# Optimization experiments

Measured on AMD Instinct MI355X. Metric: run time of the kernel, lower is better.

The kernel has to match this reference:

```python
import jax, jax.numpy as jnp
import numpy as np

EMB, NH, NG, T_MAX = 2048, 16, 4, 2048
HD = EMB // NH          # 128
HPG = NH // NG          # 4
B, T = 2, 2048


def _rope_tables(t):
    inv_freq = 1.0 / (10000.0 ** (jnp.arange(0, HD, 2, dtype=jnp.float32) / HD))
    freqs = jnp.outer(jnp.arange(t, dtype=jnp.float32), inv_freq)  # [t, HD//2]
    return jnp.cos(freqs), jnp.sin(freqs)


def _apply_rope(x, cos, sin):
    # x: [..., t, HD], interleaved pairs (0::2 real, 1::2 imag)
    x1 = x[..., 0::2]
    x2 = x[..., 1::2]
    r1 = x1 * cos - x2 * sin
    r2 = x1 * sin + x2 * cos
    return jnp.stack([r1, r2], axis=-1).reshape(x.shape)


def setup_inputs() -> dict:
    key = jax.random.key(0)
    ks = jax.random.split(key, 5)
    s = 0.02
    return {
        "x": jax.random.normal(ks[0], (B, T, EMB), dtype=jnp.float32),
        "Wq": jax.random.normal(ks[1], (EMB, EMB), dtype=jnp.float32) * s,
        "Wk": jax.random.normal(ks[2], (NG * HD, EMB), dtype=jnp.float32) * s,
        "Wv": jax.random.normal(ks[3], (NG * HD, EMB), dtype=jnp.float32) * s,
        "Wo": jax.random.normal(ks[4], (EMB, EMB), dtype=jnp.float32) * s,
    }


def reference(x, Wq, Wk, Wv, Wo):
    b, t, _ = x.shape
    cos, sin = _rope_tables(t)  # [t, HD//2] each; broadcast over batch/heads

    # projections (torch Linear: x @ W.T)
    q = (x @ Wq.T).reshape(b, t, NH, HD).transpose(0, 2, 1, 3)  # [b, NH, t, HD]
    k = (x @ Wk.T).reshape(b, t, NG, HD).transpose(0, 2, 1, 3)  # [b, NG, t, HD]
    v = (x @ Wv.T).reshape(b, t, NG, HD).transpose(0, 2, 1, 3)  # [b, NG, t, HD]

    q = _apply_rope(q, cos, sin)
    k = _apply_rope(k, cos, sin)

    # grouped attention without materializing expanded K/V
    qg = q.reshape(b, NG, HPG, t, HD)                       # [b, g, h, t, d]
    scale = 1.0 / jnp.sqrt(jnp.asarray(HD, dtype=x.dtype))
    scores = jnp.einsum('bghtd,bgsd->bghts', qg, k) * scale  # [b, g, h, t, s]

    causal = jnp.tril(jnp.ones((t, t), dtype=bool))
    scores = jnp.where(causal, scores, jnp.finfo(scores.dtype).min)
    attn = jax.nn.softmax(scores, axis=-1)

    out = jnp.einsum('bghts,bgsd->bghtd', attn, v)           # [b, g, h, t, d]
    out = out.reshape(b, NH, t, HD).transpose(0, 2, 1, 3).reshape(b, t, EMB)
    return out @ Wo.T
```

## Files before the change

kernel.cpp:

```cpp
#include <hip/hip_runtime.h>
#include <stdint.h>
#include <math.h>

#define EMB 2048
#define NHq 16
#define NGk 4
#define HD 128
#define Bb 2
#define Tt 2048
#define MROWS (Bb*Tt)
#define QKVN 3072
#define NQT 32

typedef __bf16 bf16x8 __attribute__((ext_vector_type(8)));
typedef float f32x4 __attribute__((ext_vector_type(4)));
typedef unsigned int u32x4 __attribute__((ext_vector_type(4)));
typedef unsigned short u16;
typedef unsigned int u32;

__device__ __forceinline__ u16 f2bf(float f) {
    unsigned int u = __float_as_uint(f);
    u += 0x7fff + ((u >> 16) & 1);
    return (u16)(u >> 16);
}
__device__ __forceinline__ float bf2f(u16 u) {
    return __uint_as_float(((u32)u) << 16);
}
__device__ __forceinline__ u32 cvt_pk_bf16(float lo, float hi) {
    u32 r;
    asm("v_cvt_pk_bf16_f32 %0, %1, %2" : "=v"(r) : "v"(lo), "v"(hi));
    return r;
}

#define GLOAD_LDS16(g, l) \
    __builtin_amdgcn_global_load_lds((const __attribute__((address_space(1))) void*)(g), \
                                     (__attribute__((address_space(3))) void*)(l), 16, 0, 0)
#define FENCE asm volatile("" ::: "memory")
#define BARRIER { FENCE; __builtin_amdgcn_s_barrier(); FENCE; }
#define VMCNT(n) asm volatile("s_waitcnt vmcnt(" #n ")")

__global__ void cast_bf16_kernel(const float* __restrict__ src, u16* __restrict__ dst, int n4) {
    int i = blockIdx.x * blockDim.x + threadIdx.x;
    if (i < n4) {
        float4 v = reinterpret_cast<const float4*>(src)[i];
        ushort4 o;
        o.x = f2bf(v.x); o.y = f2bf(v.y); o.z = f2bf(v.z); o.w = f2bf(v.w);
        reinterpret_cast<ushort4*>(dst)[i] = o;
    }
}

__global__ void wcast_kernel(const float* __restrict__ Wq, const float* __restrict__ Wk,
                             const float* __restrict__ Wv, const float* __restrict__ Wo,
                             u16* __restrict__ dst) {
    int i = blockIdx.x * blockDim.x + threadIdx.x;
    const float* src; int local;
    if (i < 1048576)      { src = Wq; local = i; }
    else if (i < 1310720) { src = Wk; local = i - 1048576; }
    else if (i < 1572864) { src = Wv; local = i - 1310720; }
    else                  { src = Wo; local = i - 1572864; }
    float4 v = reinterpret_cast<const float4*>(src)[local];
    ushort4 o;
    o.x = f2bf(v.x); o.y = f2bf(v.y); o.z = f2bf(v.z); o.w = f2bf(v.w);
    reinterpret_cast<ushort4*>(dst)[i] = o;
}

__global__ void rope_tables_kernel(float* __restrict__ ctab, float* __restrict__ stab) {
    int t = blockIdx.x, i = threadIdx.x;
    float inv = powf(10000.f, -2.f * (float)i / (float)HD);
    float ang = (float)t * inv;
    ctab[t * 64 + i] = cosf(ang);
    stab[t * 64 + i] = sinf(ang);
}

__global__ void rope_qk_kernel(const u16* __restrict__ lin, const float* __restrict__ ctab,
                               const float* __restrict__ stab, u16* __restrict__ Qb,
                               u16* __restrict__ Kb, float qscale) {
    int i = threadIdx.x;
    int tt = blockIdx.x * 4 + threadIdx.y;
    int hh = blockIdx.y, b = blockIdx.z;
    int coloff; u16* out; float scale;
    if (hh < NHq) { coloff = hh * HD; scale = qscale;
                    out = Qb + (((size_t)(b * NHq + hh)) * Tt + tt) * HD; }
    else { int g = hh - NHq; coloff = EMB + g * HD; scale = 1.f;
           out = Kb + (((size_t)(b * NGk + g)) * Tt + tt) * HD; }
    u32 pair = *reinterpret_cast<const u32*>(&lin[((size_t)(b * Tt + tt)) * QKVN + coloff + 2 * i]);
    float x1 = bf2f((u16)(pair & 0xffff)), x2 = bf2f((u16)(pair >> 16));
    float c = ctab[tt * 64 + i], s = stab[tt * 64 + i];
    ushort2 o;
    o.x = f2bf((x1 * c - x2 * s) * scale);
    o.y = f2bf((x1 * s + x2 * c) * scale);
    *reinterpret_cast<ushort2*>(&out[2 * i]) = o;
}

__global__ void vtrans_kernel(const u16* __restrict__ lin, u16* __restrict__ vt) {
    int tx = threadIdx.x, dy = threadIdx.y;
    int tt = blockIdx.x * 64 + tx;
    int g = blockIdx.y, b = blockIdx.z;
    int ttp = (tt & ~31) | (((tt >> 2) & 3) * 8 + ((tt >> 4) & 1) * 4 + (tt & 3));
    const u16* src = &lin[((size_t)(b * Tt + tt)) * QKVN + EMB + NGk * HD + g * HD];
    u16* dst = &vt[(((size_t)(b * NGk + g)) * HD) * Tt + ttp];
    #pragma unroll
    for (int k = 0; k < 16; ++k) {
        int d = dy + k * 8;
        dst[(size_t)d * Tt] = src[d];
    }
}

template<int OUTBF>
__global__ __launch_bounds__(256) void gemm_bt(const u16* __restrict__ A, const u16* __restrict__ W,
                                               void* __restrict__ Cout, int M, int N, int K) {
    __shared__ u16 Atile[128 * 32];
    __shared__ u16 Btile[128 * 32];
    const int brow = blockIdx.x * 128;
    const int bcol = blockIdx.y * 128;
    const int t = threadIdx.x;
    const int w = t >> 6, l = t & 63;
    const int lr = l & 15, lq = l >> 4;
    const int wr = (w >> 1) * 64, wc = (w & 1) * 64;
    f32x4 acc[4][4] = {};
    const int nkt = K >> 5;
    for (int kt = 0; kt < nkt; ++kt) {
        const int k0 = kt * 32;
        #pragma unroll
        for (int i = 0; i < 2; ++i) {
            int f = i * 256 + t;
            int row = f >> 2, cb = (f & 3) * 8;
            GLOAD_LDS16(A + (size_t)(brow + row) * K + k0 + cb, &Atile[(i * 256 + w * 64) * 8]);
            GLOAD_LDS16(W + (size_t)(bcol + row) * K + k0 + cb, &Btile[(i * 256 + w * 64) * 8]);
        }
        __syncthreads();
        bf16x8 a[4], b[4];
        #pragma unroll
        for (int m = 0; m < 4; ++m)
            a[m] = *reinterpret_cast<const bf16x8*>(&Atile[(wr + m * 16 + lr) * 32 + lq * 8]);
        #pragma unroll
        for (int n = 0; n < 4; ++n)
            b[n] = *reinterpret_cast<const bf16x8*>(&Btile[(wc + n * 16 + lr) * 32 + lq * 8]);
        #pragma unroll
        for (int m = 0; m < 4; ++m)
            #pragma unroll
            for (int n = 0; n < 4; ++n)
                acc[m][n] = __builtin_amdgcn_mfma_f32_16x16x32_bf16(a[m], b[n], acc[m][n], 0, 0, 0);
        __syncthreads();
    }
    #pragma unroll
    for (int m = 0; m < 4; ++m)
        #pragma unroll
        for (int n = 0; n < 4; ++n)
            #pragma unroll
            for (int r = 0; r < 4; ++r) {
                size_t idx = (size_t)(brow + wr + m * 16 + lq * 4 + r) * N + bcol + wc + n * 16 + lr;
                if (OUTBF) ((u16*)Cout)[idx] = f2bf(acc[m][n][r]);
                else       ((float*)Cout)[idx] = acc[m][n][r];
            }
}

template<int OUTBF>
__global__ __launch_bounds__(512) void gemm256(const u16* __restrict__ A, const u16* __restrict__ W,
                                               void* __restrict__ Cout, int M, int N, int K) {
    __shared__ __align__(16) char smem[131072];
    const int nbm = M >> 8;
    const int nwg = gridDim.x;
    const int cpx = nwg >> 3;
    const int swz = ((int)blockIdx.x & 7) * cpx + ((int)blockIdx.x >> 3);
    const int brow = (swz % nbm) << 8;
    const int bcol = (swz / nbm) << 8;
    const int t = threadIdx.x;
    const int l = t & 63, lr = l & 15, lq = l >> 4;
    const int w = t >> 6, wm = w >> 2, wn = w & 3;

    int lrj[2], slj[2], sej[2];
    #pragma unroll
    for (int j = 0; j < 2; ++j) {
        int c = j * 512 + t;
        lrj[j] = c >> 3; slj[j] = c & 7; sej[j] = (c & 7) ^ ((c >> 3) & 7);
    }

#define STGA(d, kt1, h) { \
    _Pragma("unroll") \
    for (int j = 0; j < 2; ++j) { \
        int row = (lrj[j] & 63) + (h) * 64 + (lrj[j] >> 6) * 128; \
        GLOAD_LDS16(A + (size_t)(brow + row) * K + (size_t)(kt1) * 64 + sej[j] * 8, \
                    smem + (d) * 65536 + row * 128 + slj[j] * 16); } }
#define STGB(d, kt1, h) { \
    _Pragma("unroll") \
    for (int j = 0; j < 2; ++j) { \
        int row = (lrj[j] & 31) + (h) * 32 + (lrj[j] >> 5) * 64; \
        GLOAD_LDS16(W + (size_t)(bcol + row) * K + (size_t)(kt1) * 64 + sej[j] * 8, \
                    smem + (d) * 65536 + 32768 + row * 128 + slj[j] * 16); } }
#define RDA(cur, mh) { \
    _Pragma("unroll") \
    for (int m = 0; m < 4; ++m) \
        _Pragma("unroll") \
        for (int kk = 0; kk < 2; ++kk) { \
            int row = wm * 128 + (mh) * 64 + m * 16 + lr; \
            int slr = (kk * 4 + lq) ^ (lr & 7); \
            af[m][kk] = *reinterpret_cast<const bf16x8*>(smem + (cur) * 65536 + row * 128 + slr * 16); } }
#define RDB(cur, nh, bq) { \
    _Pragma("unroll") \
    for (int n = 0; n < 2; ++n) \
        _Pragma("unroll") \
        for (int kk = 0; kk < 2; ++kk) { \
            int row = wn * 64 + (nh) * 32 + n * 16 + lr; \
            int slr = (kk * 4 + lq) ^ (lr & 7); \
            bq[n][kk] = *reinterpret_cast<const bf16x8*>(smem + (cur) * 65536 + 32768 + row * 128 + slr * 16); } }
#define MM(bq, mo, no) { \
    __builtin_amdgcn_s_setprio(1); \
    _Pragma("unroll") \
    for (int m = 0; m < 4; ++m) \
        _Pragma("unroll") \
        for (int n = 0; n < 2; ++n) \
            _Pragma("unroll") \
            for (int kk = 0; kk < 2; ++kk) \
                acc[(mo) + m][(no) + n] = __builtin_amdgcn_mfma_f32_16x16x32_bf16( \
                    af[m][kk], bq[n][kk], acc[(mo) + m][(no) + n], 0, 0, 0); \
    __builtin_amdgcn_s_setprio(0); }

    f32x4 acc[8][4] = {};
    bf16x8 af[4][2], b0[2][2], b1[2][2];
    const int nkt = K >> 6;

    STGA(0, 0, 0); STGB(0, 0, 0); STGB(0, 0, 1); STGA(0, 0, 1);
    VMCNT(4); BARRIER;

    for (int kt = 0; kt < nkt; ++kt) {
        const int cur = kt & 1, nxt = cur ^ 1;
        const bool more = (kt + 1 < nkt);
        RDA(cur, 0); RDB(cur, 0, b0);
        if (more) { STGA(nxt, kt + 1, 0); VMCNT(4); } else { VMCNT(2); }
        BARRIER;
        MM(b0, 0, 0);
        BARRIER;
        RDB(cur, 1, b1);
        if (more) { STGB(nxt, kt + 1, 0); VMCNT(4); } else { VMCNT(0); }
        BARRIER;
        MM(b1, 0, 2);
        BARRIER;
        RDA(cur, 1);
        if (more) STGB(nxt, kt + 1, 1);
        BARRIER;
        MM(b0, 4, 0);
        BARRIER;
        if (more) { STGA(nxt, kt + 1, 1); VMCNT(4); }
        BARRIER;
        MM(b1, 4, 2);
        BARRIER;
    }

    #pragma unroll
    for (int m = 0; m < 8; ++m)
        #pragma unroll
        for (int n = 0; n < 4; ++n)
            #pragma unroll
            for (int r = 0; r < 4; ++r) {
                size_t idx = (size_t)(brow + wm * 128 + m * 16 + lq * 4 + r) * N + bcol + wn * 64 + n * 16 + lr;
                if (OUTBF) ((u16*)Cout)[idx] = f2bf(acc[m][n][r]);
                else       ((float*)Cout)[idx] = acc[m][n][r];
            }
#undef STGA
#undef STGB
#undef RDA
#undef RDB
#undef MM
}

__global__ __launch_bounds__(256) void flash_attn(const u16* __restrict__ Q, const u16* __restrict__ K,
                                                  const u16* __restrict__ Vt, u16* __restrict__ Out) {
    __shared__ __align__(16) char smem[65536];
    const int h = blockIdx.y;
    const int b = blockIdx.z;
    const int qt = (b == 0) ? blockIdx.x : (15 - blockIdx.x);
    const int g = h >> 2;
    const int t = threadIdx.x;
    const int w = t >> 6, l = t & 63;
    const int lr = l & 15, lq = l >> 4;
    const int qbase = qt * 128 + w * 32;

    const size_t qhead = ((size_t)(b * NHq + h)) * Tt;
    bf16x8 qf0[4], qf1[4];
    #pragma unroll
    for (int d = 0; d < 4; ++d) {
        qf0[d] = *reinterpret_cast<const bf16x8*>(&Q[(qhead + qbase + lr) * HD + d * 32 + lq * 8]);
        qf1[d] = *reinterpret_cast<const bf16x8*>(&Q[(qhead + qbase + 16 + lr) * HD + d * 32 + lq * 8]);
    }
    bf16x8 ones;
    #pragma unroll
    for (int j = 0; j < 8; ++j) ones[j] = (__bf16)1.0f;

    f32x4 o0[8] = {}, o1[8] = {};
    f32x4 ls0 = {}, ls1 = {};

    const int q0 = qbase + lr;
    const int q1 = qbase + 16 + lr;
    const int lastvis = (qbase + 31) >> 6;
    const size_t kbase  = ((size_t)(b * NGk + g)) * Tt * HD;
    const size_t vtbase = ((size_t)(b * NGk + g)) * HD * Tt;
    const int nkt = 2 * (qt + 1);

    int kofs[4], vofs[4];
    #pragma unroll
    for (int j = 0; j < 4; ++j) {
        int krow = j * 16 + (t >> 4);
        kofs[j] = krow * HD + (((t & 15) ^ (krow & 7)) * 8);
        int vrow = j * 32 + (t >> 3);
        vofs[j] = vrow * (int)Tt + (((t & 7) ^ (vrow & 7)) * 8);
    }

    #pragma unroll
    for (int j = 0; j < 4; ++j) {
        GLOAD_LDS16(K + kbase + kofs[j], smem + (j * 256 + t) * 16);
        GLOAD_LDS16(Vt + vtbase + vofs[j], smem + 32768 + (j * 256 + t) * 16);
    }

    for (int kt = 0; kt < nkt; ++kt) {
        __syncthreads();
        if (kt + 1 < nkt) {
            const size_t kp1 = (size_t)(kt + 1) * 64;
            char* kd = smem + ((kt + 1) & 1) * 16384;
            char* vd = smem + 32768 + ((kt + 1) & 1) * 16384;
            #pragma unroll
            for (int j = 0; j < 4; ++j) {
                GLOAD_LDS16(K + kbase + kp1 * HD + kofs[j], kd + (j * 256 + t) * 16);
                GLOAD_LDS16(Vt + vtbase + kp1 + vofs[j], vd + (j * 256 + t) * 16);
            }
        }
        if (kt > lastvis) continue;
        const char* Kb = smem + (kt & 1) * 16384;
        const char* Vb = smem + 32768 + (kt & 1) * 16384;

        f32x4 s0[4] = {}, s1[4] = {};
        __builtin_amdgcn_s_setprio(1);
        #pragma unroll
        for (int ct = 0; ct < 4; ++ct) {
            #pragma unroll
            for (int d = 0; d < 4; ++d) {
                int row = ct * 16 + lr;
                int bo = row * 256 + ((d * 64 + lq * 16) ^ ((row & 7) << 4));
                bf16x8 kf = *reinterpret_cast<const bf16x8*>(Kb + bo);
                s0[ct] = __builtin_amdgcn_mfma_f32_16x16x32_bf16(kf, qf0[d], s0[ct], 0, 0, 0);
                s1[ct] = __builtin_amdgcn_mfma_f32_16x16x32_bf16(kf, qf1[d], s1[ct], 0, 0, 0);
            }
        }
        __builtin_amdgcn_s_setprio(0);

        const bool diag = (kt == lastvis);
        const int kvb = kt * 64 + lq * 4;
        bf16x8 pf0[2], pf1[2];
        {
            float e[4][4];
            #pragma unroll
            for (int ct = 0; ct < 4; ++ct)
                #pragma unroll
                for (int r = 0; r < 4; ++r)
                    e[ct][r] = exp2f(s0[ct][r]);
            if (diag) {
                #pragma unroll
                for (int ct = 0; ct < 4; ++ct)
                    #pragma unroll
                    for (int r = 0; r < 4; ++r)
                        if (kvb + ct * 16 + r > q0) e[ct][r] = 0.f;
            }
            #pragma unroll
            for (int ks = 0; ks < 2; ++ks) {
                u32x4 pk;
                pk[0] = cvt_pk_bf16(e[ks * 2][0], e[ks * 2][1]);
                pk[1] = cvt_pk_bf16(e[ks * 2][2], e[ks * 2][3]);
                pk[2] = cvt_pk_bf16(e[ks * 2 + 1][0], e[ks * 2 + 1][1]);
                pk[3] = cvt_pk_bf16(e[ks * 2 + 1][2], e[ks * 2 + 1][3]);
                pf0[ks] = __builtin_bit_cast(bf16x8, pk);
            }
        }
        {
            float e[4][4];
            #pragma unroll
            for (int ct = 0; ct < 4; ++ct)
                #pragma unroll
                for (int r = 0; r < 4; ++r)
                    e[ct][r] = exp2f(s1[ct][r]);
            if (diag) {
                #pragma unroll
                for (int ct = 0; ct < 4; ++ct)
                    #pragma unroll
                    for (int r = 0; r < 4; ++r)
                        if (kvb + ct * 16 + r > q1) e[ct][r] = 0.f;
            }
            #pragma unroll
            for (int ks = 0; ks < 2; ++ks) {
                u32x4 pk;
                pk[0] = cvt_pk_bf16(e[ks * 2][0], e[ks * 2][1]);
                pk[1] = cvt_pk_bf16(e[ks * 2][2], e[ks * 2][3]);
                pk[2] = cvt_pk_bf16(e[ks * 2 + 1][0], e[ks * 2 + 1][1]);
                pk[3] = cvt_pk_bf16(e[ks * 2 + 1][2], e[ks * 2 + 1][3]);
                pf1[ks] = __builtin_bit_cast(bf16x8, pk);
            }
        }

        __builtin_amdgcn_s_setprio(1);
        #pragma unroll
        for (int n = 0; n < 8; ++n) {
            int vrow = n * 16 + lr;
            #pragma unroll
            for (int ks = 0; ks < 2; ++ks) {
                int bv = vrow * 128 + ((ks * 64 + lq * 16) ^ ((vrow & 7) << 4));
                bf16x8 vf = *reinterpret_cast<const bf16x8*>(Vb + bv);
                o0[n] = __builtin_amdgcn_mfma_f32_16x16x32_bf16(vf, pf0[ks], o0[n], 0, 0, 0);
                o1[n] = __builtin_amdgcn_mfma_f32_16x16x32_bf16(vf, pf1[ks], o1[n], 0, 0, 0);
            }
        }
        ls0 = __builtin_amdgcn_mfma_f32_16x16x32_bf16(ones, pf0[0], ls0, 0, 0, 0);
        ls0 = __builtin_amdgcn_mfma_f32_16x16x32_bf16(ones, pf0[1], ls0, 0, 0, 0);
        ls1 = __builtin_amdgcn_mfma_f32_16x16x32_bf16(ones, pf1[0], ls1, 0, 0, 0);
        ls1 = __builtin_amdgcn_mfma_f32_16x16x32_bf16(ones, pf1[1], ls1, 0, 0, 0);
        __builtin_amdgcn_s_setprio(0);
    }

    {
        const float inv0 = 1.f / ls0[0];
        const float inv1 = 1.f / ls1[0];
        u16* out0 = Out + ((size_t)(b * Tt) + q0) * EMB + h * HD;
        u16* out1 = Out + ((size_t)(b * Tt) + q1) * EMB + h * HD;
        #pragma unroll
        for (int n = 0; n < 8; ++n) {
            uint2 p0, p1;
            p0.x = cvt_pk_bf16(o0[n][0] * inv0, o0[n][1] * inv0);
            p0.y = cvt_pk_bf16(o0[n][2] * inv0, o0[n][3] * inv0);
            p1.x = cvt_pk_bf16(o1[n][0] * inv1, o1[n][1] * inv1);
            p1.y = cvt_pk_bf16(o1[n][2] * inv1, o1[n][3] * inv1);
            *reinterpret_cast<uint2*>(&out0[n * 16 + lq * 4]) = p0;
            *reinterpret_cast<uint2*>(&out1[n * 16 + lq * 4]) = p1;
        }
    }
}

extern "C" void kernel_launch(void* const* d_in, const int* in_sizes, int n_in,
                              void* d_out, int out_size, void* d_ws, size_t ws_size,
                              hipStream_t stream) {
    (void)in_sizes; (void)n_in; (void)out_size; (void)ws_size;
    const float* x  = (const float*)d_in[0];
    const float* Wq = (const float*)d_in[1];
    const float* Wk = (const float*)d_in[2];
    const float* Wv = (const float*)d_in[3];
    const float* Wo = (const float*)d_in[4];
    float* out = (float*)d_out;

    char* ws = (char*)d_ws;
    size_t off = 0;
    auto alloc = [&](size_t bytes) { char* p = ws + off; off += (bytes + 255) & ~(size_t)255; return p; };

    u16* w_bf    = (u16*)alloc((size_t)(QKVN * EMB + EMB * EMB) * 2);
    u16* x_bf    = (u16*)alloc((size_t)MROWS * EMB * 2);
    u16* qkv_lin = (u16*)alloc((size_t)MROWS * QKVN * 4);
    u16* Qb      = (u16*)alloc((size_t)Bb * NHq * Tt * HD * 2);
    u16* Kb      = (u16*)alloc((size_t)Bb * NGk * Tt * HD * 2);
    u16* Vtb     = (u16*)alloc((size_t)Bb * NGk * HD * Tt * 2);
    float* ctab  = (float*)alloc((size_t)Tt * 64 * 4);
    float* stab  = (float*)alloc((size_t)Tt * 64 * 4);
    u16* attnout = qkv_lin;

    u16* wo_bf = w_bf + (size_t)QKVN * EMB;

    cast_bf16_kernel<<<(MROWS * EMB / 4 + 255) / 256, 256, 0, stream>>>(x, x_bf, MROWS * EMB / 4);
    wcast_kernel<<<(QKVN * EMB + EMB * EMB) / 4 / 256, 256, 0, stream>>>(Wq, Wk, Wv, Wo, w_bf);
    rope_tables_kernel<<<Tt, 64, 0, stream>>>(ctab, stab);

    gemm256<1><<<dim3((MROWS / 256) * (QKVN / 256)), 512, 0, stream>>>(x_bf, w_bf, qkv_lin, MROWS, QKVN, EMB);

    const float qscale = 1.44269504088896f / sqrtf((float)HD);
    rope_qk_kernel<<<dim3(Tt / 4, NHq + NGk, Bb), dim3(64, 4), 0, stream>>>(qkv_lin, ctab, stab, Qb, Kb, qscale);
    vtrans_kernel<<<dim3(Tt / 64, NGk, Bb), dim3(64, 8), 0, stream>>>(qkv_lin, Vtb);

    flash_attn<<<dim3(16, NHq, Bb), 256, 0, stream>>>(Qb, Kb, Vtb, attnout);

    gemm_bt<0><<<dim3(MROWS / 128, EMB / 128), 256, 0, stream>>>(attnout, wo_bf, out, MROWS, EMB, EMB);
}
```

Measured before the change: 221.6 us.

## Pair low and high 64-row query tiles per block to balance causal attention work

Each attention block now handles two 64-row query tiles, a low tile and its mirror high tile (index 31-ilo), instead of one contiguous 128-row tile. The block streams K/V up to the high tile's diagonal and skips the low tile's MFMAs and softmax once past its own diagonal. This evens out the causal triangle across blocks and removes whole-wave idle iterations. In exchange it adds per-iteration branches on lo_act, and each wave now covers only 16 rows per tile, which can cost register pressure and some divergence.

```diff
diff --git a/kernel.cpp b/kernel.cpp
--- a/kernel.cpp
+++ b/kernel.cpp
@@ -269,33 +269,32 @@
     __shared__ __align__(16) char smem[65536];
     const int h = blockIdx.y;
     const int b = blockIdx.z;
-    const int qt = (b == 0) ? blockIdx.x : (15 - blockIdx.x);
+    const int ilo = (b == 0) ? blockIdx.x : (15 - blockIdx.x);
+    const int ihi = NQT - 1 - ilo;
     const int g = h >> 2;
     const int t = threadIdx.x;
     const int w = t >> 6, l = t & 63;
     const int lr = l & 15, lq = l >> 4;
-    const int qbase = qt * 128 + w * 32;
 
     const size_t qhead = ((size_t)(b * NHq + h)) * Tt;
-    bf16x8 qf0[4], qf1[4];
+    bf16x8 qfl[4], qfh[4];
     #pragma unroll
     for (int d = 0; d < 4; ++d) {
-        qf0[d] = *reinterpret_cast<const bf16x8*>(&Q[(qhead + qbase + lr) * HD + d * 32 + lq * 8]);
-        qf1[d] = *reinterpret_cast<const bf16x8*>(&Q[(qhead + qbase + 16 + lr) * HD + d * 32 + lq * 8]);
+        qfl[d] = *reinterpret_cast<const bf16x8*>(&Q[(qhead + ilo * 64 + w * 16 + lr) * HD + d * 32 + lq * 8]);
+        qfh[d] = *reinterpret_cast<const bf16x8*>(&Q[(qhead + ihi * 64 + w * 16 + lr) * HD + d * 32 + lq * 8]);
     }
     bf16x8 ones;
     #pragma unroll
     for (int j = 0; j < 8; ++j) ones[j] = (__bf16)1.0f;
 
-    f32x4 o0[8] = {}, o1[8] = {};
-    f32x4 ls0 = {}, ls1 = {};
-
-    const int q0 = qbase + lr;
-    const int q1 = qbase + 16 + lr;
-    const int lastvis = (qbase + 31) >> 6;
+    f32x4 ol[8] = {}, oh[8] = {};
+    f32x4 lsl = {}, lsh = {};
+
+    const int qlo = ilo * 64 + w * 16 + lr;
+    const int qhi = ihi * 64 + w * 16 + lr;
     const size_t kbase  = ((size_t)(b * NGk + g)) * Tt * HD;
     const size_t vtbase = ((size_t)(b * NGk + g)) * HD * Tt;
-    const int nkt = 2 * (qt + 1);
+    const int nkt = ihi + 1;
 
     int kofs[4], vofs[4];
     #pragma unroll
@@ -324,11 +323,11 @@
                 GLOAD_LDS16(Vt + vtbase + kp1 + vofs[j], vd + (j * 256 + t) * 16);
             }
         }
-        if (kt > lastvis) continue;
         const char* Kb = smem + (kt & 1) * 16384;
         const char* Vb = smem + 32768 + (kt & 1) * 16384;
-
-        f32x4 s0[4] = {}, s1[4] = {};
+        const bool lo_act = (kt <= ilo);
+
+        f32x4 sl[4] = {}, sh[4] = {};
         __builtin_amdgcn_s_setprio(1);
         #pragma unroll
         for (int ct = 0; ct < 4; ++ct) {
@@ -337,28 +336,27 @@
                 int row = ct * 16 + lr;
                 int bo = row * 256 + ((d * 64 + lq * 16) ^ ((row & 7) << 4));
                 bf16x8 kf = *reinterpret_cast<const bf16x8*>(Kb + bo);
-                s0[ct] = __builtin_amdgcn_mfma_f32_16x16x32_bf16(kf, qf0[d], s0[ct], 0, 0, 0);
-                s1[ct] = __builtin_amdgcn_mfma_f32_16x16x32_bf16(kf, qf1[d], s1[ct], 0, 0, 0);
+                sh[ct] = __builtin_amdgcn_mfma_f32_16x16x32_bf16(kf, qfh[d], sh[ct], 0, 0, 0);
+                if (lo_act) sl[ct] = __builtin_amdgcn_mfma_f32_16x16x32_bf16(kf, qfl[d], sl[ct], 0, 0, 0);
             }
         }
         __builtin_amdgcn_s_setprio(0);
 
-        const bool diag = (kt == lastvis);
         const int kvb = kt * 64 + lq * 4;
-        bf16x8 pf0[2], pf1[2];
+        bf16x8 pfh[2], pfl[2];
         {
             float e[4][4];
             #pragma unroll
             for (int ct = 0; ct < 4; ++ct)
                 #pragma unroll
                 for (int r = 0; r < 4; ++r)
-                    e[ct][r] = exp2f(s0[ct][r]);
-            if (diag) {
+                    e[ct][r] = exp2f(sh[ct][r]);
+            if (kt == nkt - 1) {
                 #pragma unroll
                 for (int ct = 0; ct < 4; ++ct)
                     #pragma unroll
                     for (int r = 0; r < 4; ++r)
-                        if (kvb + ct * 16 + r > q0) e[ct][r] = 0.f;
+                        if (kvb + ct * 16 + r > qhi) e[ct][r] = 0.f;
             }
             #pragma unroll
             for (int ks = 0; ks < 2; ++ks) {
@@ -367,22 +365,22 @@
                 pk[1] = cvt_pk_bf16(e[ks * 2][2], e[ks * 2][3]);
                 pk[2] = cvt_pk_bf16(e[ks * 2 + 1][0], e[ks * 2 + 1][1]);
                 pk[3] = cvt_pk_bf16(e[ks * 2 + 1][2], e[ks * 2 + 1][3]);
-                pf0[ks] = __builtin_bit_cast(bf16x8, pk);
-            }
-        }
-        {
+                pfh[ks] = __builtin_bit_cast(bf16x8, pk);
+            }
+        }
+        if (lo_act) {
             float e[4][4];
             #pragma unroll
             for (int ct = 0; ct < 4; ++ct)
                 #pragma unroll
                 for (int r = 0; r < 4; ++r)
-                    e[ct][r] = exp2f(s1[ct][r]);
-            if (diag) {
+                    e[ct][r] = exp2f(sl[ct][r]);
+            if (kt == ilo) {
                 #pragma unroll
                 for (int ct = 0; ct < 4; ++ct)
                     #pragma unroll
                     for (int r = 0; r < 4; ++r)
-                        if (kvb + ct * 16 + r > q1) e[ct][r] = 0.f;
+                        if (kvb + ct * 16 + r > qlo) e[ct][r] = 0.f;
             }
             #pragma unroll
             for (int ks = 0; ks < 2; ++ks) {
@@ -391,7 +389,7 @@
                 pk[1] = cvt_pk_bf16(e[ks * 2][2], e[ks * 2][3]);
                 pk[2] = cvt_pk_bf16(e[ks * 2 + 1][0], e[ks * 2 + 1][1]);
                 pk[3] = cvt_pk_bf16(e[ks * 2 + 1][2], e[ks * 2 + 1][3]);
-                pf1[ks] = __builtin_bit_cast(bf16x8, pk);
+                pfl[ks] = __builtin_bit_cast(bf16x8, pk);
             }
         }
 
@@ -403,31 +401,33 @@
             for (int ks = 0; ks < 2; ++ks) {
                 int bv = vrow * 128 + ((ks * 64 + lq * 16) ^ ((vrow & 7) << 4));
                 bf16x8 vf = *reinterpret_cast<const bf16x8*>(Vb + bv);
-                o0[n] = __builtin_amdgcn_mfma_f32_16x16x32_bf16(vf, pf0[ks], o0[n], 0, 0, 0);
-                o1[n] = __builtin_amdgcn_mfma_f32_16x16x32_bf16(vf, pf1[ks], o1[n], 0, 0, 0);
-            }
-        }
-        ls0 = __builtin_amdgcn_mfma_f32_16x16x32_bf16(ones, pf0[0], ls0, 0, 0, 0);
-        ls0 = __builtin_amdgcn_mfma_f32_16x16x32_bf16(ones, pf0[1], ls0, 0, 0, 0);
-        ls1 = __builtin_amdgcn_mfma_f32_16x16x32_bf16(ones, pf1[0], ls1, 0, 0, 0);
-        ls1 = __builtin_amdgcn_mfma_f32_16x16x32_bf16(ones, pf1[1], ls1, 0, 0, 0);
+                oh[n] = __builtin_amdgcn_mfma_f32_16x16x32_bf16(vf, pfh[ks], oh[n], 0, 0, 0);
+                if (lo_act) ol[n] = __builtin_amdgcn_mfma_f32_16x16x32_bf16(vf, pfl[ks], ol[n], 0, 0, 0);
+            }
+        }
+        lsh = __builtin_amdgcn_mfma_f32_16x16x32_bf16(ones, pfh[0], lsh, 0, 0, 0);
+        lsh = __builtin_amdgcn_mfma_f32_16x16x32_bf16(ones, pfh[1], lsh, 0, 0, 0);
+        if (lo_act) {
+            lsl = __builtin_amdgcn_mfma_f32_16x16x32_bf16(ones, pfl[0], lsl, 0, 0, 0);
+            lsl = __builtin_amdgcn_mfma_f32_16x16x32_bf16(ones, pfl[1], lsl, 0, 0, 0);
+        }
         __builtin_amdgcn_s_setprio(0);
     }
 
     {
-        const float inv0 = 1.f / ls0[0];
-        const float inv1 = 1.f / ls1[0];
-        u16* out0 = Out + ((size_t)(b * Tt) + q0) * EMB + h * HD;
-        u16* out1 = Out + ((size_t)(b * Tt) + q1) * EMB + h * HD;
+        const float invh = 1.f / lsh[0];
+        const float invl = 1.f / lsl[0];
+        u16* outh = Out + ((size_t)(b * Tt) + qhi) * EMB + h * HD;
+        u16* outl = Out + ((size_t)(b * Tt) + qlo) * EMB + h * HD;
         #pragma unroll
         for (int n = 0; n < 8; ++n) {
-            uint2 p0, p1;
-            p0.x = cvt_pk_bf16(o0[n][0] * inv0, o0[n][1] * inv0);
-            p0.y = cvt_pk_bf16(o0[n][2] * inv0, o0[n][3] * inv0);
-            p1.x = cvt_pk_bf16(o1[n][0] * inv1, o1[n][1] * inv1);
-            p1.y = cvt_pk_bf16(o1[n][2] * inv1, o1[n][3] * inv1);
-            *reinterpret_cast<uint2*>(&out0[n * 16 + lq * 4]) = p0;
-            *reinterpret_cast<uint2*>(&out1[n * 16 + lq * 4]) = p1;
+            uint2 ph, pl;
+            ph.x = cvt_pk_bf16(oh[n][0] * invh, oh[n][1] * invh);
+            ph.y = cvt_pk_bf16(oh[n][2] * invh, oh[n][3] * invh);
+            pl.x = cvt_pk_bf16(ol[n][0] * invl, ol[n][1] * invl);
+            pl.y = cvt_pk_bf16(ol[n][2] * invl, ol[n][3] * invl);
+            *reinterpret_cast<uint2*>(&outh[n * 16 + lq * 4]) = ph;
+            *reinterpret_cast<uint2*>(&outl[n * 16 + lq * 4]) = pl;
         }
     }
 }
```

After: 233.4 us. +5.3%, slower.

## Switch flash attention MFMA tiles from 16x16x32 to 32x32x16

Applied to the files above, without the earlier changes.

Rewrites the flash-attention inner loops to use 32x32x16 bf16 MFMA instructions, with each wave handling a 32-query tile as one accumulator instead of two 16-row tiles. The V-transpose permutation and the causal-mask and output index mapping are changed to match the new MFMA register layout. The aim is fewer MFMA issues and fewer LDS fragment reads per K/V tile. In exchange, output stores become narrower (32-bit per lane) and the new layouts carry a correctness risk.

```diff
diff --git a/kernel.cpp b/kernel.cpp
--- a/kernel.cpp
+++ b/kernel.cpp
@@ -14,6 +14,7 @@
 
 typedef __bf16 bf16x8 __attribute__((ext_vector_type(8)));
 typedef float f32x4 __attribute__((ext_vector_type(4)));
+typedef float f32x16 __attribute__((ext_vector_type(16)));
 typedef unsigned int u32x4 __attribute__((ext_vector_type(4)));
 typedef unsigned short u16;
 typedef unsigned int u32;
@@ -96,7 +97,7 @@
     int tx = threadIdx.x, dy = threadIdx.y;
     int tt = blockIdx.x * 64 + tx;
     int g = blockIdx.y, b = blockIdx.z;
-    int ttp = (tt & ~31) | (((tt >> 2) & 3) * 8 + ((tt >> 4) & 1) * 4 + (tt & 3));
+    int ttp = (tt & ~15) | ((tt & 3) + 4 * ((tt >> 3) & 1) + 8 * ((tt >> 2) & 1));
     const u16* src = &lin[((size_t)(b * Tt + tt)) * QKVN + EMB + NGk * HD + g * HD];
     u16* dst = &vt[(((size_t)(b * NGk + g)) * HD) * Tt + ttp];
     #pragma unroll
@@ -273,25 +274,23 @@
     const int g = h >> 2;
     const int t = threadIdx.x;
     const int w = t >> 6, l = t & 63;
-    const int lr = l & 15, lq = l >> 4;
+    const int lh = l >> 5;
+    const int lc = l & 31;
     const int qbase = qt * 128 + w * 32;
+    const int q = qbase + lc;
 
     const size_t qhead = ((size_t)(b * NHq + h)) * Tt;
-    bf16x8 qf0[4], qf1[4];
-    #pragma unroll
-    for (int d = 0; d < 4; ++d) {
-        qf0[d] = *reinterpret_cast<const bf16x8*>(&Q[(qhead + qbase + lr) * HD + d * 32 + lq * 8]);
-        qf1[d] = *reinterpret_cast<const bf16x8*>(&Q[(qhead + qbase + 16 + lr) * HD + d * 32 + lq * 8]);
-    }
+    bf16x8 qf[8];
+    #pragma unroll
+    for (int ds = 0; ds < 8; ++ds)
+        qf[ds] = *reinterpret_cast<const bf16x8*>(&Q[(qhead + q) * HD + ds * 16 + lh * 8]);
     bf16x8 ones;
     #pragma unroll
     for (int j = 0; j < 8; ++j) ones[j] = (__bf16)1.0f;
 
-    f32x4 o0[8] = {}, o1[8] = {};
-    f32x4 ls0 = {}, ls1 = {};
-
-    const int q0 = qbase + lr;
-    const int q1 = qbase + 16 + lr;
+    f32x16 o[4] = {};
+    f32x16 lsum = {};
+
     const int lastvis = (qbase + 31) >> 6;
     const size_t kbase  = ((size_t)(b * NGk + g)) * Tt * HD;
     const size_t vtbase = ((size_t)(b * NGk + g)) * HD * Tt;
@@ -305,7 +304,6 @@
         int vrow = j * 32 + (t >> 3);
         vofs[j] = vrow * (int)Tt + (((t & 7) ^ (vrow & 7)) * 8);
     }
-
     #pragma unroll
     for (int j = 0; j < 4; ++j) {
         GLOAD_LDS16(K + kbase + kofs[j], smem + (j * 256 + t) * 16);
@@ -328,107 +326,73 @@
         const char* Kb = smem + (kt & 1) * 16384;
         const char* Vb = smem + 32768 + (kt & 1) * 16384;
 
-        f32x4 s0[4] = {}, s1[4] = {};
+        f32x16 s0 = {}, s1 = {};
         __builtin_amdgcn_s_setprio(1);
         #pragma unroll
-        for (int ct = 0; ct < 4; ++ct) {
-            #pragma unroll
-            for (int d = 0; d < 4; ++d) {
-                int row = ct * 16 + lr;
-                int bo = row * 256 + ((d * 64 + lq * 16) ^ ((row & 7) << 4));
-                bf16x8 kf = *reinterpret_cast<const bf16x8*>(Kb + bo);
-                s0[ct] = __builtin_amdgcn_mfma_f32_16x16x32_bf16(kf, qf0[d], s0[ct], 0, 0, 0);
-                s1[ct] = __builtin_amdgcn_mfma_f32_16x16x32_bf16(kf, qf1[d], s1[ct], 0, 0, 0);
-            }
+        for (int ds = 0; ds < 8; ++ds) {
+            int r0 = lc;
+            int bo0 = r0 * 256 + ((ds * 32 + lh * 16) ^ ((r0 & 7) << 4));
+            bf16x8 kf0 = *reinterpret_cast<const bf16x8*>(Kb + bo0);
+            s0 = __builtin_amdgcn_mfma_f32_32x32x16_bf16(kf0, qf[ds], s0, 0, 0, 0);
+            int r1 = 32 + lc;
+            int bo1 = r1 * 256 + ((ds * 32 + lh * 16) ^ ((r1 & 7) << 4));
+            bf16x8 kf1 = *reinterpret_cast<const bf16x8*>(Kb + bo1);
+            s1 = __builtin_amdgcn_mfma_f32_32x32x16_bf16(kf1, qf[ds], s1, 0, 0, 0);
         }
         __builtin_amdgcn_s_setprio(0);
 
-        const bool diag = (kt == lastvis);
-        const int kvb = kt * 64 + lq * 4;
-        bf16x8 pf0[2], pf1[2];
-        {
-            float e[4][4];
-            #pragma unroll
-            for (int ct = 0; ct < 4; ++ct)
-                #pragma unroll
-                for (int r = 0; r < 4; ++r)
-                    e[ct][r] = exp2f(s0[ct][r]);
-            if (diag) {
-                #pragma unroll
-                for (int ct = 0; ct < 4; ++ct)
-                    #pragma unroll
-                    for (int r = 0; r < 4; ++r)
-                        if (kvb + ct * 16 + r > q0) e[ct][r] = 0.f;
-            }
-            #pragma unroll
-            for (int ks = 0; ks < 2; ++ks) {
-                u32x4 pk;
-                pk[0] = cvt_pk_bf16(e[ks * 2][0], e[ks * 2][1]);
-                pk[1] = cvt_pk_bf16(e[ks * 2][2], e[ks * 2][3]);
-                pk[2] = cvt_pk_bf16(e[ks * 2 + 1][0], e[ks * 2 + 1][1]);
-                pk[3] = cvt_pk_bf16(e[ks * 2 + 1][2], e[ks * 2 + 1][3]);
-                pf0[ks] = __builtin_bit_cast(bf16x8, pk);
-            }
-        }
-        {
-            float e[4][4];
-            #pragma unroll
-            for (int ct = 0; ct < 4; ++ct)
-                #pragma unroll
-                for (int r = 0; r < 4; ++r)
-                    e[ct][r] = exp2f(s1[ct][r]);
-            if (diag) {
-                #pragma unroll
-                for (int ct = 0; ct < 4; ++ct)
-                    #pragma unroll
-                    for (int r = 0; r < 4; ++r)
-                        if (kvb + ct * 16 + r > q1) e[ct][r] = 0.f;
-            }
-            #pragma unroll
-            for (int ks = 0; ks < 2; ++ks) {
-                u32x4 pk;
-                pk[0] = cvt_pk_bf16(e[ks * 2][0], e[ks * 2][1]);
-                pk[1] = cvt_pk_bf16(e[ks * 2][2], e[ks * 2][3]);
-                pk[2] = cvt_pk_bf16(e[ks * 2 + 1][0], e[ks * 2 + 1][1]);
-                pk[3] = cvt_pk_bf16(e[ks * 2 + 1][2], e[ks * 2 + 1][3]);
-                pf1[ks] = __builtin_bit_cast(bf16x8, pk);
-            }
+        float e0[16], e1[16];
+        #pragma unroll
+        for (int r = 0; r < 16; ++r) { e0[r] = exp2f(s0[r]); e1[r] = exp2f(s1[r]); }
+        if (kt == lastvis) {
+            #pragma unroll
+            for (int r = 0; r < 16; ++r) {
+                int kv0 = kt * 64 + (r & 3) + 8 * (r >> 2) + 4 * lh;
+                if (kv0 > q) e0[r] = 0.f;
+                if (kv0 + 32 > q) e1[r] = 0.f;
+            }
+        }
+        bf16x8 pf[4];
+        #pragma unroll
+        for (int ks = 0; ks < 4; ++ks) {
+            const float* x = (ks >= 2) ? e1 : e0;
+            const int j = (ks & 1) * 8;
+            u32x4 pk;
+            pk[0] = cvt_pk_bf16(x[j], x[j + 1]);
+            pk[1] = cvt_pk_bf16(x[j + 2], x[j + 3]);
+            pk[2] = cvt_pk_bf16(x[j + 4], x[j + 5]);
+            pk[3] = cvt_pk_bf16(x[j + 6], x[j + 7]);
+            pf[ks] = __builtin_bit_cast(bf16x8, pk);
         }
 
         __builtin_amdgcn_s_setprio(1);
         #pragma unroll
-        for (int n = 0; n < 8; ++n) {
-            int vrow = n * 16 + lr;
-            #pragma unroll
-            for (int ks = 0; ks < 2; ++ks) {
-                int bv = vrow * 128 + ((ks * 64 + lq * 16) ^ ((vrow & 7) << 4));
+        for (int vd = 0; vd < 4; ++vd) {
+            int d = vd * 32 + lc;
+            #pragma unroll
+            for (int ks = 0; ks < 4; ++ks) {
+                int bv = d * 128 + ((ks * 32 + lh * 16) ^ ((d & 7) << 4));
                 bf16x8 vf = *reinterpret_cast<const bf16x8*>(Vb + bv);
-                o0[n] = __builtin_amdgcn_mfma_f32_16x16x32_bf16(vf, pf0[ks], o0[n], 0, 0, 0);
-                o1[n] = __builtin_amdgcn_mfma_f32_16x16x32_bf16(vf, pf1[ks], o1[n], 0, 0, 0);
-            }
-        }
-        ls0 = __builtin_amdgcn_mfma_f32_16x16x32_bf16(ones, pf0[0], ls0, 0, 0, 0);
-        ls0 = __builtin_amdgcn_mfma_f32_16x16x32_bf16(ones, pf0[1], ls0, 0, 0, 0);
-        ls1 = __builtin_amdgcn_mfma_f32_16x16x32_bf16(ones, pf1[0], ls1, 0, 0, 0);
-        ls1 = __builtin_amdgcn_mfma_f32_16x16x32_bf16(ones, pf1[1], ls1, 0, 0, 0);
+                o[vd] = __builtin_amdgcn_mfma_f32_32x32x16_bf16(vf, pf[ks], o[vd], 0, 0, 0);
+            }
+        }
+        #pragma unroll
+        for (int ks = 0; ks < 4; ++ks)
+            lsum = __builtin_amdgcn_mfma_f32_32x32x16_bf16(ones, pf[ks], lsum, 0, 0, 0);
         __builtin_amdgcn_s_setprio(0);
     }
 
     {
-        const float inv0 = 1.f / ls0[0];
-        const float inv1 = 1.f / ls1[0];
-        u16* out0 = Out + ((size_t)(b * Tt) + q0) * EMB + h * HD;
-        u16* out1 = Out + ((size_t)(b * Tt) + q1) * EMB + h * HD;
-        #pragma unroll
-        for (int n = 0; n < 8; ++n) {
-            uint2 p0, p1;
-            p0.x = cvt_pk_bf16(o0[n][0] * inv0, o0[n][1] * inv0);
-            p0.y = cvt_pk_bf16(o0[n][2] * inv0, o0[n][3] * inv0);
-            p1.x = cvt_pk_bf16(o1[n][0] * inv1, o1[n][1] * inv1);
-            p1.y = cvt_pk_bf16(o1[n][2] * inv1, o1[n][3] * inv1);
-            *reinterpret_cast<uint2*>(&out0[n * 16 + lq * 4]) = p0;
-            *reinterpret_cast<uint2*>(&out1[n * 16 + lq * 4]) = p1;
-        }
+        const float inv = 1.f / lsum[0];
+        u16* outp = Out + ((size_t)(b * Tt) + q) * EMB + h * HD;
+        #pragma unroll
+        for (int vd = 0; vd < 4; ++vd)
+            #pragma unroll
+            for (int i = 0; i < 8; ++i) {
+                const int r = 2 * i;
+                const int d = vd * 32 + (r & 3) + 8 * (r >> 2) + 4 * lh;
+                *reinterpret_cast<u32*>(&outp[d]) = cvt_pk_bf16(o[vd][r] * inv, o[vd][r + 1] * inv);
+            }
     }
 }
 
```

New measurement: 251.8 us. 13.6% more time.
